# Kernel tuning notes

Hardware: AMD Instinct MI355X
Metric: run time of the kernel (lower is better)

## Reference

```python
import jax, jax.numpy as jnp
import numpy as np

N_NODES = 16384
N_EDGES = 131072
EDGE_DIM = 16
IN_CH = 32
OUT_CH = 32
HID_EDGE = 64
MLP_HID = 64  # int(32 * 2.0)
OUT_FINAL = 10
N_GRAPHS = 64
BN_EPS = 1e-5


def setup_inputs() -> dict:
    key = jax.random.key(0)
    ks = jax.random.split(key, 20)
    s = lambda *sh: 1.0 / np.sqrt(sh[0])
    inp = {
        'x': jax.random.normal(ks[0], (N_NODES, IN_CH), jnp.float32),
        'edge_attr': jax.random.normal(ks[1], (N_EDGES, EDGE_DIM), jnp.float32),
        'edge_index': jax.random.randint(ks[2], (2, N_EDGES), 0, N_NODES, jnp.int64),
        'batch': jnp.sort(jax.random.randint(ks[3], (N_NODES,), 0, N_GRAPHS, jnp.int64)),
    }
    # layer 0: edge MLP (EDGE_DIM->HID_EDGE->IN_CH*OUT_CH), root, bias, BN affine
    inp['w1_0'] = jax.random.normal(ks[4], (EDGE_DIM, HID_EDGE), jnp.float32) * s(EDGE_DIM)
    inp['b1_0'] = jnp.zeros((HID_EDGE,), jnp.float32)
    inp['w2_0'] = jax.random.normal(ks[5], (HID_EDGE, IN_CH * OUT_CH), jnp.float32) * s(HID_EDGE)
    inp['b2_0'] = jnp.zeros((IN_CH * OUT_CH,), jnp.float32)
    inp['root_0'] = jax.random.normal(ks[6], (IN_CH, OUT_CH), jnp.float32) * s(IN_CH)
    inp['bias_0'] = jnp.zeros((OUT_CH,), jnp.float32)
    inp['gamma_0'] = jnp.ones((OUT_CH,), jnp.float32)
    inp['beta_0'] = jnp.zeros((OUT_CH,), jnp.float32)
    # layer 1: edge MLP (EDGE_DIM->HID_EDGE->OUT_CH*OUT_CH)
    inp['w1_1'] = jax.random.normal(ks[7], (EDGE_DIM, HID_EDGE), jnp.float32) * s(EDGE_DIM)
    inp['b1_1'] = jnp.zeros((HID_EDGE,), jnp.float32)
    inp['w2_1'] = jax.random.normal(ks[8], (HID_EDGE, OUT_CH * OUT_CH), jnp.float32) * s(HID_EDGE)
    inp['b2_1'] = jnp.zeros((OUT_CH * OUT_CH,), jnp.float32)
    inp['root_1'] = jax.random.normal(ks[9], (OUT_CH, OUT_CH), jnp.float32) * s(OUT_CH)
    inp['bias_1'] = jnp.zeros((OUT_CH,), jnp.float32)
    inp['gamma_1'] = jnp.ones((OUT_CH,), jnp.float32)
    inp['beta_1'] = jnp.zeros((OUT_CH,), jnp.float32)
    # final MLP (dropout is identity in eval / deterministic reference)
    inp['mlp_w1'] = jax.random.normal(ks[10], (OUT_CH, MLP_HID), jnp.float32) * s(OUT_CH)
    inp['mlp_b1'] = jnp.zeros((MLP_HID,), jnp.float32)
    inp['mlp_w2'] = jax.random.normal(ks[11], (MLP_HID, OUT_FINAL), jnp.float32) * s(MLP_HID)
    inp['mlp_b2'] = jnp.zeros((OUT_FINAL,), jnp.float32)
    return inp


def _nnconv(x, src, dst, edge_attr, w1, b1, w2, b2, root, bias, out_ch):
    # per-edge weight matrices from the edge MLP: [E, in, out]
    h = jax.nn.relu(edge_attr @ w1 + b1)
    W = (h @ w2 + b2).reshape(-1, x.shape[1], out_ch)
    msg = jnp.einsum('ei,eio->eo', x[src], W)  # gather + per-edge matmul
    agg = jax.ops.segment_sum(msg, dst, num_segments=N_NODES)
    cnt = jax.ops.segment_sum(jnp.ones((dst.shape[0], 1), x.dtype), dst, num_segments=N_NODES)
    agg = agg / jnp.maximum(cnt, 1.0)  # scatter-mean (zero-degree nodes -> 0)
    return agg + x @ root + bias


def _bn(x, gamma, beta):
    m = jnp.mean(x, axis=0)
    v = jnp.var(x, axis=0)
    return (x - m) * jax.lax.rsqrt(v + BN_EPS) * gamma + beta


def reference(x, edge_attr, edge_index, batch,
              w1_0, b1_0, w2_0, b2_0, root_0, bias_0, gamma_0, beta_0,
              w1_1, b1_1, w2_1, b2_1, root_1, bias_1, gamma_1, beta_1,
              mlp_w1, mlp_b1, mlp_w2, mlp_b2):
    src, dst = edge_index[0], edge_index[1]
    h = _nnconv(x, src, dst, edge_attr, w1_0, b1_0, w2_0, b2_0, root_0, bias_0, OUT_CH)
    h = jax.nn.relu(_bn(h, gamma_0, beta_0))
    h = _nnconv(h, src, dst, edge_attr, w1_1, b1_1, w2_1, b2_1, root_1, bias_1, OUT_CH)
    h = jax.nn.relu(_bn(h, gamma_1, beta_1))
    # global mean pool over graphs
    pooled = jax.ops.segment_sum(h, batch, num_segments=N_GRAPHS)
    gcnt = jax.ops.segment_sum(jnp.ones((h.shape[0], 1), h.dtype), batch, num_segments=N_GRAPHS)
    pooled = pooled / jnp.maximum(gcnt, 1.0)
    logits = jax.nn.relu(pooled @ mlp_w1 + mlp_b1) @ mlp_w2 + mlp_b2
    return logits
```

## Files before the change

kernel.cpp:

```cpp
#include <hip/hip_runtime.h>
#include <hip/hip_bf16.h>

#define NN 16384
#define NE 131072
#define NG 64
#define EPB 128

typedef unsigned short u16;
typedef unsigned int u32;
typedef __attribute__((ext_vector_type(8))) short short8;
typedef __attribute__((ext_vector_type(4))) float f32x4;
typedef __attribute__((ext_vector_type(2))) float f32x2;

__device__ __forceinline__ float bf2f(u16 u) {
    u32 x = ((u32)u) << 16;
    return __builtin_bit_cast(float, x);
}
__device__ __forceinline__ u16 f2bf(float f) {
    u32 u = __builtin_bit_cast(u32, f);
    u = u + 0x7fffu + ((u >> 16) & 1u);
    return (u16)(u >> 16);
}
__device__ __forceinline__ u32 pk2bf(float a, float b) {
    return (u32)f2bf(a) | ((u32)f2bf(b) << 16);
}
#if __has_builtin(__builtin_amdgcn_cvt_pk_bf16_f32)
__device__ __forceinline__ u32 pk2bf_fast(float a, float b) {
    auto v = __builtin_amdgcn_cvt_pk_bf16_f32(a, b);
    static_assert(sizeof(v) == 4, "cvt_pk_bf16 size");
    return __builtin_bit_cast(u32, v);
}
#else
__device__ __forceinline__ u32 pk2bf_fast(float a, float b) {
    u32 ua = __builtin_bit_cast(u32, a) + 0x8000u;
    u32 ub = __builtin_bit_cast(u32, b) + 0x8000u;
    return __builtin_amdgcn_perm(ub, ua, 0x07060302u);
}
#endif
__device__ __forceinline__ float loadF(const void* p, int i, bool bf) {
    return bf ? bf2f(((const u16*)p)[i]) : ((const float*)p)[i];
}
__device__ __forceinline__ int loadI(const void* p, int i, bool i64) {
    return i64 ? (int)((const long long*)p)[i] : ((const int*)p)[i];
}
__device__ __forceinline__ bool det_bf(const void* g0) {
    return ((const u16*)g0)[0] == 0x3F80u;
}
__device__ __forceinline__ bool det_i64(const void* eidx) {
    const u32* u = (const u32*)eidx;
    return (u[1] | u[3] | u[5] | u[7]) == 0u;
}

__global__ __launch_bounds__(256) void k_prep(const void* w2a, const void* b2a,
                                              const void* w2b, const void* b2b,
                                              const void* w1a, const void* w1b,
                                              u16* bp0, u16* bp1, u16* w1p0, u16* w1p1,
                                              const void* eidx, float* cnt, const void* g0) {
    const bool bf = det_bf(g0);
    int id = blockIdx.x * 256 + threadIdx.x;
    if (id < 2 * 66560) {
        int l = id / 66560, v = id % 66560;
        int j = v & 7, lane = (v >> 3) & 63, nt = (v >> 9) & 1, t = v >> 10;
        int kk = (lane >> 4) * 8 + j;
        int n = (lane & 15) + 16 * nt;
        const void* w2 = l ? w2b : w2a;
        const void* b2 = l ? b2b : b2a;
        float val = (t < 64) ? loadF(w2, t * 1024 + kk * 32 + n, bf)
                             : loadF(b2, kk * 32 + n, bf);
        (l ? bp1 : bp0)[v] = f2bf(val);
    } else if (id < 2 * 66560 + 2 * 2048) {
        int v = id - 2 * 66560;
        int l = v >> 11; v &= 2047;
        int j = v & 7, lane = (v >> 3) & 63, nt = v >> 9;
        int k = (lane >> 4) * 8 + j;
        int n = nt * 16 + (lane & 15);
        const void* w1 = l ? w1b : w1a;
        float val = (k < 16) ? loadF(w1, k * 64 + n, bf) : 0.f;
        (l ? w1p1 : w1p0)[v] = f2bf(val);
    } else {
        const bool i64 = det_i64(eidx);
        int e = id - (2 * 66560 + 2 * 2048);
        int d = loadI(eidx, NE + e, i64);
        atomicAdd(&cnt[d], 1.0f);
    }
}

#define HSTR 72
__global__ __launch_bounds__(256, 4) void k_edge(const void* ea, const u16* w1p, const void* b1,
                                                 const void* xv, int x_f32,
                                                 const void* eidx, const u16* Bpack,
                                                 float* agg, const void* g0) {
    const bool bf = det_bf(g0);
    const bool i64 = det_i64(eidx);
    __shared__ __align__(16) u16 hl[EPB * HSTR];
    const int tid = threadIdx.x;
    const int e0 = blockIdx.x * EPB;
    const int lane = tid & 63;
    const int w = tid >> 6;
    const int q = lane >> 4;
    const int m = lane & 15;
    const int wbl = w * 32;
    const int wb = e0 + wbl;

    {
        short8 Ah[2];
#pragma unroll
        for (int e2 = 0; e2 < 2; e2++) {
            int eg = wb + e2 * 16 + m;
            uint4 av = make_uint4(0u, 0u, 0u, 0u);
            if (bf) {
                uint4 t = *(const uint4*)((const char*)ea + (size_t)eg * 32 + (q & 1) * 16);
                if (q < 2) av = t;
            } else {
                const float4* p = (const float4*)((const char*)ea + (size_t)eg * 64 + (q & 1) * 32);
                float4 a = p[0], b = p[1];
                if (q < 2) av = make_uint4(pk2bf_fast(a.x, a.y), pk2bf_fast(a.z, a.w),
                                           pk2bf_fast(b.x, b.y), pk2bf_fast(b.z, b.w));
            }
            Ah[e2] = __builtin_bit_cast(short8, av);
        }
#pragma unroll
        for (int nt = 0; nt < 4; nt++) {
            uint4 bw = *(const uint4*)&w1p[(nt * 64 + lane) * 8];
            short8 Bf = __builtin_bit_cast(short8, bw);
            float bb = loadF(b1, nt * 16 + m, bf);
#pragma unroll
            for (int e2 = 0; e2 < 2; e2++) {
                f32x4 c = __builtin_amdgcn_mfma_f32_16x16x32_bf16(
                    Ah[e2], Bf, f32x4{0.f, 0.f, 0.f, 0.f}, 0, 0, 0);
                int rbase = (wbl + e2 * 16 + q * 4) * HSTR + nt * 16 + m;
#pragma unroll
                for (int r = 0; r < 4; r++) {
                    u32 pkd = pk2bf_fast(fmaxf(c[r] + bb, 0.f), 0.f);
                    hl[rbase + r * HSTR] = (u16)pkd;
                }
            }
        }
    }

    const bool xf = (x_f32 != 0) || (!bf);
    f32x2 xr2[2][4];
#pragma unroll
    for (int mt = 0; mt < 2; mt++) {
        int s = loadI(eidx, wb + mt * 16 + m, i64);
        if (xf) {
            const float4* xp = (const float4*)xv + (size_t)s * 8 + q * 2;
            float4 a = xp[0], b = xp[1];
            xr2[mt][0] = f32x2{a.x, a.y}; xr2[mt][1] = f32x2{a.z, a.w};
            xr2[mt][2] = f32x2{b.x, b.y}; xr2[mt][3] = f32x2{b.z, b.w};
        } else {
            const uint4* xp = (const uint4*)((const char*)xv + (size_t)s * 64 + q * 16);
            uint4 a = *xp;
            xr2[mt][0] = f32x2{bf2f((u16)(a.x & 0xffff)), bf2f((u16)(a.x >> 16))};
            xr2[mt][1] = f32x2{bf2f((u16)(a.y & 0xffff)), bf2f((u16)(a.y >> 16))};
            xr2[mt][2] = f32x2{bf2f((u16)(a.z & 0xffff)), bf2f((u16)(a.z >> 16))};
            xr2[mt][3] = f32x2{bf2f((u16)(a.w & 0xffff)), bf2f((u16)(a.w >> 16))};
        }
    }

    const uint4* bp4 = (const uint4*)Bpack;
    uint4 pb[4][2];
#pragma unroll
    for (int d = 0; d < 4; d++) {
        pb[d][0] = bp4[(d * 2 + 0) * 64 + lane];
        pb[d][1] = bp4[(d * 2 + 1) * 64 + lane];
    }

    __syncthreads();

    f32x4 acc[2][2];
#pragma unroll
    for (int mt = 0; mt < 2; mt++) {
        acc[mt][0] = f32x4{0.f, 0.f, 0.f, 0.f};
        acc[mt][1] = f32x4{0.f, 0.f, 0.f, 0.f};
    }
    int rowb[2];
#pragma unroll
    for (int mt = 0; mt < 2; mt++) rowb[mt] = (wbl + mt * 16 + m) * HSTR;

    for (int tc = 0; tc < 8; tc++) {
        uint4 hb[2];
        hb[0] = *(const uint4*)&hl[rowb[0] + tc * 8];
        hb[1] = *(const uint4*)&hl[rowb[1] + tc * 8];
#pragma unroll
        for (int tj = 0; tj < 8; tj++) {
            int t = tc * 8 + tj;
            int slot = tj & 3;
            uint4 bu0 = pb[slot][0], bu1 = pb[slot][1];
            int tn = t + 4; if (tn > 64) tn = 64;
            pb[slot][0] = bp4[(tn * 2 + 0) * 64 + lane];
            pb[slot][1] = bp4[(tn * 2 + 1) * 64 + lane];
            short8 B0 = __builtin_bit_cast(short8, bu0);
            short8 B1 = __builtin_bit_cast(short8, bu1);
#pragma unroll
            for (int mt = 0; mt < 2; mt++) {
                u32 wd = ((const u32*)&hb[mt])[tj >> 1];
                u32 hbits = (tj & 1) ? (wd & 0xFFFF0000u) : (wd << 16);
                float hs = __builtin_bit_cast(float, hbits);
                f32x2 h2 = {hs, hs};
                f32x2 p0 = h2 * xr2[mt][0];
                f32x2 p1 = h2 * xr2[mt][1];
                f32x2 p2 = h2 * xr2[mt][2];
                f32x2 p3 = h2 * xr2[mt][3];
                uint4 au = make_uint4(pk2bf_fast(p0.x, p0.y), pk2bf_fast(p1.x, p1.y),
                                      pk2bf_fast(p2.x, p2.y), pk2bf_fast(p3.x, p3.y));
                short8 A = __builtin_bit_cast(short8, au);
                acc[mt][0] = __builtin_amdgcn_mfma_f32_16x16x32_bf16(A, B0, acc[mt][0], 0, 0, 0);
                acc[mt][1] = __builtin_amdgcn_mfma_f32_16x16x32_bf16(A, B1, acc[mt][1], 0, 0, 0);
            }
        }
    }
    {
        short8 B0 = __builtin_bit_cast(short8, pb[0][0]);
        short8 B1 = __builtin_bit_cast(short8, pb[0][1]);
#pragma unroll
        for (int mt = 0; mt < 2; mt++) {
            uint4 au = make_uint4(pk2bf_fast(xr2[mt][0].x, xr2[mt][0].y),
                                  pk2bf_fast(xr2[mt][1].x, xr2[mt][1].y),
                                  pk2bf_fast(xr2[mt][2].x, xr2[mt][2].y),
                                  pk2bf_fast(xr2[mt][3].x, xr2[mt][3].y));
            short8 A = __builtin_bit_cast(short8, au);
            acc[mt][0] = __builtin_amdgcn_mfma_f32_16x16x32_bf16(A, B0, acc[mt][0], 0, 0, 0);
            acc[mt][1] = __builtin_amdgcn_mfma_f32_16x16x32_bf16(A, B1, acc[mt][1], 0, 0, 0);
        }
    }

#pragma unroll
    for (int mt = 0; mt < 2; mt++) {
        int eb = wb + mt * 16 + q * 4;
#pragma unroll
        for (int r = 0; r < 4; r++) {
            int dst = loadI(eidx, NE + eb + r, i64);
            float* ap = agg + (size_t)dst * 32 + m;
            atomicAdd(ap, acc[mt][0][r]);
            atomicAdd(ap + 16, acc[mt][1][r]);
        }
    }
}

__global__ __launch_bounds__(256) void k_node(const float* agg, const float* cnt,
                                              const void* xv, int x_f32,
                                              const void* root, const void* bias,
                                              float* hpre, float* sS, float* sQ,
                                              const void* g0) {
    const bool bf = det_bf(g0);
    const int tid = threadIdx.x;
    const int v = blockIdx.x * 8 + (tid >> 5);
    const int o = tid & 31;
    const bool xf = (x_f32 != 0) || (!bf);
    float xrow[32];
    if (xf) {
        const float* x = (const float*)xv + (size_t)v * 32;
#pragma unroll
        for (int i = 0; i < 32; i++) xrow[i] = x[i];
    } else {
        const u16* x = (const u16*)xv + (size_t)v * 32;
#pragma unroll
        for (int i = 0; i < 32; i++) xrow[i] = bf2f(x[i]);
    }
    float a;
    if (bf) {
        const u16* R = (const u16*)root;
        a = bf2f(((const u16*)bias)[o]);
#pragma unroll
        for (int i = 0; i < 32; i++) a += xrow[i] * bf2f(R[i * 32 + o]);
    } else {
        const float* R = (const float*)root;
        a = ((const float*)bias)[o];
#pragma unroll
        for (int i = 0; i < 32; i++) a += xrow[i] * R[i * 32 + o];
    }
    float pre = agg[(size_t)v * 32 + o] / fmaxf(cnt[v], 1.0f) + a;
    hpre[(size_t)v * 32 + o] = pre;

    __shared__ float lS[256], lQ[256];
    lS[tid] = pre;
    lQ[tid] = pre * pre;
    __syncthreads();
#pragma unroll
    for (int off = 128; off >= 32; off >>= 1) {
        if (tid < off) { lS[tid] += lS[tid + off]; lQ[tid] += lQ[tid + off]; }
        __syncthreads();
    }
    if (tid < 32) {
        int slot = (blockIdx.x & 15) * 32 + tid;
        atomicAdd(&sS[slot], lS[tid]);
        atomicAdd(&sQ[slot], lQ[tid]);
    }
}

__global__ __launch_bounds__(256) void k_bn(const float* hpre, const float* sS, const float* sQ,
                                            const void* gamma, const void* beta, float* hout,
                                            const void* g0) {
    const bool bf = det_bf(g0);
    const int tid = threadIdx.x;
    const int v = blockIdx.x * 8 + (tid >> 5);
    const int o = tid & 31;
    float s = 0.f, qq = 0.f;
#pragma unroll
    for (int p = 0; p < 16; p++) { s += sS[p * 32 + o]; qq += sQ[p * 32 + o]; }
    float mn = s * (1.0f / 16384.0f);
    float var = qq * (1.0f / 16384.0f) - mn * mn;
    float inv = rsqrtf(var + 1e-5f);
    float g = loadF(gamma, o, bf), b = loadF(beta, o, bf);
    float y = (hpre[(size_t)v * 32 + o] - mn) * inv * g + b;
    hout[(size_t)v * 32 + o] = fmaxf(y, 0.f);
}

__global__ __launch_bounds__(256) void k_bnpool(const float* hpre, const float* sS, const float* sQ,
                                                const void* gamma, const void* beta,
                                                const void* batch, float* pooled, float* gcnt,
                                                const void* eidx, const void* g0) {
    const bool bf = det_bf(g0);
    const bool i64 = det_i64(eidx);
    const int tid = threadIdx.x;
    const int o = tid & 31;
    const int c = tid >> 5;
    float s = 0.f, qq = 0.f;
#pragma unroll
    for (int p = 0; p < 16; p++) { s += sS[p * 32 + o]; qq += sQ[p * 32 + o]; }
    float mn = s * (1.0f / 16384.0f);
    float var = qq * (1.0f / 16384.0f) - mn * mn;
    float inv = rsqrtf(var + 1e-5f);
    float gg = loadF(gamma, o, bf), bb = loadF(beta, o, bf);

    const int base = blockIdx.x * 256 + c;
    float acc = 0.f, cacc = 0.f;
    int curg = -1;
#pragma unroll 4
    for (int j = 0; j < 32; j++) {
        int v = base + j * 8;
        int g = loadI(batch, v, i64);
        float y = fmaxf((hpre[(size_t)v * 32 + o] - mn) * inv * gg + bb, 0.f);
        if (g != curg) {
            if (curg >= 0) {
                atomicAdd(&pooled[curg * 32 + o], acc);
                if (o == 0) atomicAdd(&gcnt[curg], cacc);
            }
            acc = 0.f; cacc = 0.f; curg = g;
        }
        acc += y; cacc += 1.f;
    }
    if (curg >= 0) {
        atomicAdd(&pooled[curg * 32 + o], acc);
        if (o == 0) atomicAdd(&gcnt[curg], cacc);
    }
}

__global__ __launch_bounds__(64) void k_final(const float* pooled, const float* gcnt,
                        const void* w1, const void* b1, const void* w2, const void* b2,
                        void* out, const void* g0) {
    const bool bf = det_bf(g0);
    const int g = blockIdx.x;
    const int j = threadIdx.x;
    float inv = 1.0f / fmaxf(gcnt[g], 1.0f);
    float a = loadF(b1, j, bf);
#pragma unroll
    for (int i = 0; i < 32; i++) {
        float p = pooled[g * 32 + i] * inv;
        a += p * loadF(w1, i * 64 + j, bf);
    }
    a = fmaxf(a, 0.f);
    float lg[10];
#pragma unroll
    for (int c = 0; c < 10; c++) lg[c] = a * loadF(w2, j * 10 + c, bf);
#pragma unroll
    for (int off = 32; off >= 1; off >>= 1) {
#pragma unroll
        for (int c = 0; c < 10; c++) lg[c] += __shfl_down(lg[c], off, 64);
    }
    if (j == 0) {
        if (bf) {
            u16* op = (u16*)out;
#pragma unroll
            for (int c = 0; c < 10; c++) op[g * 10 + c] = f2bf(lg[c] + loadF(b2, c, bf));
        } else {
            float* op = (float*)out;
#pragma unroll
            for (int c = 0; c < 10; c++) op[g * 10 + c] = lg[c] + loadF(b2, c, bf);
        }
    }
}

extern "C" void kernel_launch(void* const* d_in, const int* in_sizes, int n_in,
                              void* d_out, int out_size, void* d_ws, size_t ws_size,
                              hipStream_t stream) {
    char* ws = (char*)d_ws;
    u16* bp0  = (u16*)(ws + 256);
    u16* bp1  = (u16*)(ws + 256 + 133120);
    u16* w1p0 = (u16*)(ws + 266496);
    u16* w1p1 = (u16*)(ws + 270592);
    char* zbase = ws + 274688;
    float* agg    = (float*)(zbase);
    float* cnt    = (float*)(zbase + 2097152);
    float* sS0    = (float*)(zbase + 2162688);
    float* sQ0    = (float*)(zbase + 2164736);
    float* sS1    = (float*)(zbase + 2166784);
    float* sQ1    = (float*)(zbase + 2168832);
    float* pooled = (float*)(zbase + 2170880);
    float* gcnt   = (float*)(zbase + 2179072);
    const size_t zsize = 2179328;
    float* hpre = (float*)(ws + 274688 + 2179328);
    float* hout = (float*)(ws + 274688 + 2179328 + 2097152);

    const void* x     = d_in[0];
    const void* ea    = d_in[1];
    const void* eidx  = d_in[2];
    const void* batch = d_in[3];
    const void* g0    = d_in[10];

    (void)hipMemsetAsync(zbase, 0, zsize, stream);
    k_prep<<<1048, 256, 0, stream>>>(d_in[6], d_in[7], d_in[14], d_in[15],
                                     d_in[4], d_in[12],
                                     bp0, bp1, w1p0, w1p1, eidx, cnt, g0);

    k_edge<<<NE / EPB, 256, 0, stream>>>(ea, w1p0, d_in[5], x, 0, eidx, bp0, agg, g0);
    k_node<<<NN / 8, 256, 0, stream>>>(agg, cnt, x, 0, d_in[8], d_in[9], hpre, sS0, sQ0, g0);
    k_bn<<<NN / 8, 256, 0, stream>>>(hpre, sS0, sQ0, d_in[10], d_in[11], hout, g0);

    (void)hipMemsetAsync(agg, 0, 2097152, stream);

    k_edge<<<NE / EPB, 256, 0, stream>>>(ea, w1p1, d_in[13], hout, 1, eidx, bp1, agg, g0);
    k_node<<<NN / 8, 256, 0, stream>>>(agg, cnt, hout, 1, d_in[16], d_in[17], hpre, sS1, sQ1, g0);

    k_bnpool<<<NN / 256, 256, 0, stream>>>(hpre, sS1, sQ1, d_in[18], d_in[19], batch,
                                           pooled, gcnt, eidx, g0);
    k_final<<<NG, 64, 0, stream>>>(pooled, gcnt, d_in[20], d_in[21], d_in[22], d_in[23], d_out, g0);
}
```

Measured before the change: 223.1 us.

## Fuse BN+ReLU into layer-1 gather, stage edge weights in LDS, drop memset

Removes the standalone BatchNorm kernel: layer-1 edge and node kernels recompute the per-channel BN scale/shift from the partial sums and apply BN+ReLU to gathered pre-activations on the fly. Node kernel zeroes agg after reading, eliminating the second memset. The edge kernel now stages the packed second-layer weights through shared memory in 1024-uint4 chunks per tc step with register prefetch, replacing per-lane global prefetches. This adds two barriers per chunk and extra LDS usage (16KB), which may lower occupancy.

New measurement: 260.5 us. 1.17x slower.

```diff
diff --git a/kernel.cpp b/kernel.cpp
--- a/kernel.cpp
+++ b/kernel.cpp
@@ -87,12 +87,16 @@
 
 #define HSTR 72
 __global__ __launch_bounds__(256, 4) void k_edge(const void* ea, const u16* w1p, const void* b1,
-                                                 const void* xv, int x_f32,
+                                                 const void* xv, int layer1,
+                                                 const float* sSp, const float* sQp,
+                                                 const void* gammap, const void* betap,
                                                  const void* eidx, const u16* Bpack,
                                                  float* agg, const void* g0) {
     const bool bf = det_bf(g0);
     const bool i64 = det_i64(eidx);
     __shared__ __align__(16) u16 hl[EPB * HSTR];
+    __shared__ __align__(16) uint4 Bs[1024];
+    __shared__ __align__(16) float bnS[32], bnB[32];
     const int tid = threadIdx.x;
     const int e0 = blockIdx.x * EPB;
     const int lane = tid & 63;
@@ -101,6 +105,23 @@
     const int m = lane & 15;
     const int wbl = w * 32;
     const int wb = e0 + wbl;
+
+    const uint4* bp4 = (const uint4*)Bpack;
+    uint4 st[4];
+#pragma unroll
+    for (int i = 0; i < 4; i++) st[i] = bp4[i * 256 + tid];
+
+    if (layer1 && tid < 32) {
+        float s = 0.f, qq = 0.f;
+#pragma unroll
+        for (int p = 0; p < 16; p++) { s += sSp[p * 32 + tid]; qq += sQp[p * 32 + tid]; }
+        float mn = s * (1.0f / 16384.0f);
+        float var = qq * (1.0f / 16384.0f) - mn * mn;
+        float inv = rsqrtf(var + 1e-5f);
+        float g = loadF(gammap, tid, bf), b = loadF(betap, tid, bf);
+        bnS[tid] = inv * g;
+        bnB[tid] = b - mn * inv * g;
+    }
 
     {
         short8 Ah[2];
@@ -138,35 +159,51 @@
         }
     }
 
-    const bool xf = (x_f32 != 0) || (!bf);
-    f32x2 xr2[2][4];
+    float4 ga[2], gb[2];
 #pragma unroll
     for (int mt = 0; mt < 2; mt++) {
         int s = loadI(eidx, wb + mt * 16 + m, i64);
-        if (xf) {
+        if (layer1 || !bf) {
             const float4* xp = (const float4*)xv + (size_t)s * 8 + q * 2;
-            float4 a = xp[0], b = xp[1];
-            xr2[mt][0] = f32x2{a.x, a.y}; xr2[mt][1] = f32x2{a.z, a.w};
-            xr2[mt][2] = f32x2{b.x, b.y}; xr2[mt][3] = f32x2{b.z, b.w};
+            ga[mt] = xp[0]; gb[mt] = xp[1];
         } else {
             const uint4* xp = (const uint4*)((const char*)xv + (size_t)s * 64 + q * 16);
             uint4 a = *xp;
-            xr2[mt][0] = f32x2{bf2f((u16)(a.x & 0xffff)), bf2f((u16)(a.x >> 16))};
-            xr2[mt][1] = f32x2{bf2f((u16)(a.y & 0xffff)), bf2f((u16)(a.y >> 16))};
-            xr2[mt][2] = f32x2{bf2f((u16)(a.z & 0xffff)), bf2f((u16)(a.z >> 16))};
-            xr2[mt][3] = f32x2{bf2f((u16)(a.w & 0xffff)), bf2f((u16)(a.w >> 16))};
-        }
-    }
-
-    const uint4* bp4 = (const uint4*)Bpack;
-    uint4 pb[4][2];
-#pragma unroll
-    for (int d = 0; d < 4; d++) {
-        pb[d][0] = bp4[(d * 2 + 0) * 64 + lane];
-        pb[d][1] = bp4[(d * 2 + 1) * 64 + lane];
-    }
+            ga[mt] = make_float4(bf2f((u16)(a.x & 0xffff)), bf2f((u16)(a.x >> 16)),
+                                 bf2f((u16)(a.y & 0xffff)), bf2f((u16)(a.y >> 16)));
+            gb[mt] = make_float4(bf2f((u16)(a.z & 0xffff)), bf2f((u16)(a.z >> 16)),
+                                 bf2f((u16)(a.w & 0xffff)), bf2f((u16)(a.w >> 16)));
+        }
+    }
+    uint4 bb0 = bp4[8192 + lane], bb1 = bp4[8256 + lane];
+
+#pragma unroll
+    for (int i = 0; i < 4; i++) Bs[i * 256 + tid] = st[i];
+#pragma unroll
+    for (int i = 0; i < 4; i++) st[i] = bp4[1024 + i * 256 + tid];
 
     __syncthreads();
+
+    f32x2 xr2[2][4];
+    if (layer1) {
+        float4 s0 = *(const float4*)&bnS[q * 8], s1 = *(const float4*)&bnS[q * 8 + 4];
+        float4 h0 = *(const float4*)&bnB[q * 8], h1 = *(const float4*)&bnB[q * 8 + 4];
+#pragma unroll
+        for (int mt = 0; mt < 2; mt++) {
+            xr2[mt][0] = f32x2{fmaxf(ga[mt].x * s0.x + h0.x, 0.f), fmaxf(ga[mt].y * s0.y + h0.y, 0.f)};
+            xr2[mt][1] = f32x2{fmaxf(ga[mt].z * s0.z + h0.z, 0.f), fmaxf(ga[mt].w * s0.w + h0.w, 0.f)};
+            xr2[mt][2] = f32x2{fmaxf(gb[mt].x * s1.x + h1.x, 0.f), fmaxf(gb[mt].y * s1.y + h1.y, 0.f)};
+            xr2[mt][3] = f32x2{fmaxf(gb[mt].z * s1.z + h1.z, 0.f), fmaxf(gb[mt].w * s1.w + h1.w, 0.f)};
+        }
+    } else {
+#pragma unroll
+        for (int mt = 0; mt < 2; mt++) {
+            xr2[mt][0] = f32x2{ga[mt].x, ga[mt].y};
+            xr2[mt][1] = f32x2{ga[mt].z, ga[mt].w};
+            xr2[mt][2] = f32x2{gb[mt].x, gb[mt].y};
+            xr2[mt][3] = f32x2{gb[mt].z, gb[mt].w};
+        }
+    }
 
     f32x4 acc[2][2];
 #pragma unroll
@@ -184,14 +221,8 @@
         hb[1] = *(const uint4*)&hl[rowb[1] + tc * 8];
 #pragma unroll
         for (int tj = 0; tj < 8; tj++) {
-            int t = tc * 8 + tj;
-            int slot = tj & 3;
-            uint4 bu0 = pb[slot][0], bu1 = pb[slot][1];
-            int tn = t + 4; if (tn > 64) tn = 64;
-            pb[slot][0] = bp4[(tn * 2 + 0) * 64 + lane];
-            pb[slot][1] = bp4[(tn * 2 + 1) * 64 + lane];
-            short8 B0 = __builtin_bit_cast(short8, bu0);
-            short8 B1 = __builtin_bit_cast(short8, bu1);
+            short8 B0 = __builtin_bit_cast(short8, Bs[(tj * 2 + 0) * 64 + lane]);
+            short8 B1 = __builtin_bit_cast(short8, Bs[(tj * 2 + 1) * 64 + lane]);
 #pragma unroll
             for (int mt = 0; mt < 2; mt++) {
                 u32 wd = ((const u32*)&hb[mt])[tj >> 1];
@@ -209,10 +240,20 @@
                 acc[mt][1] = __builtin_amdgcn_mfma_f32_16x16x32_bf16(A, B1, acc[mt][1], 0, 0, 0);
             }
         }
+        if (tc < 7) {
+            __syncthreads();
+#pragma unroll
+            for (int i = 0; i < 4; i++) Bs[i * 256 + tid] = st[i];
+            if (tc < 6) {
+#pragma unroll
+                for (int i = 0; i < 4; i++) st[i] = bp4[(tc + 2) * 1024 + i * 256 + tid];
+            }
+            __syncthreads();
+        }
     }
     {
-        short8 B0 = __builtin_bit_cast(short8, pb[0][0]);
-        short8 B1 = __builtin_bit_cast(short8, pb[0][1]);
+        short8 B0 = __builtin_bit_cast(short8, bb0);
+        short8 B1 = __builtin_bit_cast(short8, bb1);
 #pragma unroll
         for (int mt = 0; mt < 2; mt++) {
             uint4 au = make_uint4(pk2bf_fast(xr2[mt][0].x, xr2[mt][0].y),
@@ -238,8 +279,10 @@
     }
 }
 
-__global__ __launch_bounds__(256) void k_node(const float* agg, const float* cnt,
-                                              const void* xv, int x_f32,
+__global__ __launch_bounds__(256) void k_node(float* agg, const float* cnt,
+                                              const void* xv, int layer1,
+                                              const float* sSp, const float* sQp,
+                                              const void* gammap, const void* betap,
                                               const void* root, const void* bias,
                                               float* hpre, float* sS, float* sQ,
                                               const void* g0) {
@@ -247,9 +290,27 @@
     const int tid = threadIdx.x;
     const int v = blockIdx.x * 8 + (tid >> 5);
     const int o = tid & 31;
-    const bool xf = (x_f32 != 0) || (!bf);
+    __shared__ float bnS[32], bnB[32];
+    if (layer1) {
+        if (tid < 32) {
+            float s = 0.f, qq = 0.f;
+#pragma unroll
+            for (int p = 0; p < 16; p++) { s += sSp[p * 32 + tid]; qq += sQp[p * 32 + tid]; }
+            float mn = s * (1.0f / 16384.0f);
+            float var = qq * (1.0f / 16384.0f) - mn * mn;
+            float inv = rsqrtf(var + 1e-5f);
+            float g = loadF(gammap, tid, bf), b = loadF(betap, tid, bf);
+            bnS[tid] = inv * g;
+            bnB[tid] = b - mn * inv * g;
+        }
+        __syncthreads();
+    }
     float xrow[32];
-    if (xf) {
+    if (layer1) {
+        const float* x = (const float*)xv + (size_t)v * 32;
+#pragma unroll
+        for (int i = 0; i < 32; i++) xrow[i] = fmaxf(x[i] * bnS[i] + bnB[i], 0.f);
+    } else if (!bf) {
         const float* x = (const float*)xv + (size_t)v * 32;
 #pragma unroll
         for (int i = 0; i < 32; i++) xrow[i] = x[i];
@@ -270,7 +331,9 @@
 #pragma unroll
         for (int i = 0; i < 32; i++) a += xrow[i] * R[i * 32 + o];
     }
-    float pre = agg[(size_t)v * 32 + o] / fmaxf(cnt[v], 1.0f) + a;
+    float av = agg[(size_t)v * 32 + o];
+    agg[(size_t)v * 32 + o] = 0.f;
+    float pre = av / fmaxf(cnt[v], 1.0f) + a;
     hpre[(size_t)v * 32 + o] = pre;
 
     __shared__ float lS[256], lQ[256];
@@ -287,24 +350,6 @@
         atomicAdd(&sS[slot], lS[tid]);
         atomicAdd(&sQ[slot], lQ[tid]);
     }
-}
-
-__global__ __launch_bounds__(256) void k_bn(const float* hpre, const float* sS, const float* sQ,
-                                            const void* gamma, const void* beta, float* hout,
-                                            const void* g0) {
-    const bool bf = det_bf(g0);
-    const int tid = threadIdx.x;
-    const int v = blockIdx.x * 8 + (tid >> 5);
-    const int o = tid & 31;
-    float s = 0.f, qq = 0.f;
-#pragma unroll
-    for (int p = 0; p < 16; p++) { s += sS[p * 32 + o]; qq += sQ[p * 32 + o]; }
-    float mn = s * (1.0f / 16384.0f);
-    float var = qq * (1.0f / 16384.0f) - mn * mn;
-    float inv = rsqrtf(var + 1e-5f);
-    float g = loadF(gamma, o, bf), b = loadF(beta, o, bf);
-    float y = (hpre[(size_t)v * 32 + o] - mn) * inv * g + b;
-    hout[(size_t)v * 32 + o] = fmaxf(y, 0.f);
 }
 
 __global__ __launch_bounds__(256) void k_bnpool(const float* hpre, const float* sS, const float* sQ,
@@ -400,8 +445,8 @@
     float* pooled = (float*)(zbase + 2170880);
     float* gcnt   = (float*)(zbase + 2179072);
     const size_t zsize = 2179328;
-    float* hpre = (float*)(ws + 274688 + 2179328);
-    float* hout = (float*)(ws + 274688 + 2179328 + 2097152);
+    float* hpre0 = (float*)(ws + 274688 + 2179328);
+    float* hpre1 = (float*)(ws + 274688 + 2179328 + 2097152);
 
     const void* x     = d_in[0];
     const void* ea    = d_in[1];
@@ -414,16 +459,21 @@
                                      d_in[4], d_in[12],
                                      bp0, bp1, w1p0, w1p1, eidx, cnt, g0);
 
-    k_edge<<<NE / EPB, 256, 0, stream>>>(ea, w1p0, d_in[5], x, 0, eidx, bp0, agg, g0);
-    k_node<<<NN / 8, 256, 0, stream>>>(agg, cnt, x, 0, d_in[8], d_in[9], hpre, sS0, sQ0, g0);
-    k_bn<<<NN / 8, 256, 0, stream>>>(hpre, sS0, sQ0, d_in[10], d_in[11], hout, g0);
-
-    (void)hipMemsetAsync(agg, 0, 2097152, stream);
-
-    k_edge<<<NE / EPB, 256, 0, stream>>>(ea, w1p1, d_in[13], hout, 1, eidx, bp1, agg, g0);
-    k_node<<<NN / 8, 256, 0, stream>>>(agg, cnt, hout, 1, d_in[16], d_in[17], hpre, sS1, sQ1, g0);
-
-    k_bnpool<<<NN / 256, 256, 0, stream>>>(hpre, sS1, sQ1, d_in[18], d_in[19], batch,
+    k_edge<<<NE / EPB, 256, 0, stream>>>(ea, w1p0, d_in[5], x, 0,
+                                         nullptr, nullptr, nullptr, nullptr,
+                                         eidx, bp0, agg, g0);
+    k_node<<<NN / 8, 256, 0, stream>>>(agg, cnt, x, 0,
+                                       nullptr, nullptr, nullptr, nullptr,
+                                       d_in[8], d_in[9], hpre0, sS0, sQ0, g0);
+
+    k_edge<<<NE / EPB, 256, 0, stream>>>(ea, w1p1, d_in[13], hpre0, 1,
+                                         sS0, sQ0, d_in[10], d_in[11],
+                                         eidx, bp1, agg, g0);
+    k_node<<<NN / 8, 256, 0, stream>>>(agg, cnt, hpre0, 1,
+                                       sS0, sQ0, d_in[10], d_in[11],
+                                       d_in[16], d_in[17], hpre1, sS1, sQ1, g0);
+
+    k_bnpool<<<NN / 256, 256, 0, stream>>>(hpre1, sS1, sQ1, d_in[18], d_in[19], batch,
                                            pooled, gcnt, eidx, g0);
     k_final<<<NG, 64, 0, stream>>>(pooled, gcnt, d_in[20], d_in[21], d_in[22], d_in[23], d_out, g0);
 }
```
